# Performance work log

Hardware: AMD Instinct MI355X
Metric: run time of the kernel (lower is better)

Reference implementation:

```python
import jax, jax.numpy as jnp
import numpy as np

B, S, IN, OUT = 64, 512, 256, 256   # batch, seq_len, in/out features
R, NB, E = 40, 3, 262144            # num_rels, num_bases, num_edges
N = B * S                           # total nodes in batched graph


def setup_inputs() -> dict:
    key = jax.random.key(0)
    ks = jax.random.split(key, 6)
    text = jax.random.normal(ks[0], (B, S, IN), jnp.float32)
    src = jax.random.randint(ks[1], (E,), 0, N)
    dst = jax.random.randint(ks[2], (E,), 0, N)
    rel = jax.random.randint(ks[3], (E,), 0, R)
    bases = jax.random.normal(ks[4], (NB, IN, OUT), jnp.float32) / np.sqrt(IN).astype(np.float32)
    comp = jax.random.normal(ks[5], (R, NB), jnp.float32)
    bias = jnp.zeros((OUT,), jnp.float32)
    return dict(text=text, src=src, dst=dst, rel=rel, bases=bases, comp=comp, bias=bias)


def reference(text, src, dst, rel, bases, comp, bias):
    Bt, St, INt = text.shape
    h = text.reshape(-1, INt)                       # [N, in] flattened node feats
    n_nodes = h.shape[0]
    # project every node through every basis once: [N, num_bases, out]
    t = jnp.einsum('ni,bio->nbo', h, bases)
    # per-edge message: sum_b comp[rel_e, b] * (h_src @ basis_b)  -> [E, out]
    msg = jnp.einsum('eb,ebo->eo', comp[rel], t[src])
    # scatter-sum aggregation to destination nodes
    agg = jax.ops.segment_sum(msg, dst, num_segments=n_nodes)   # [N, out]
    out = jax.nn.relu(agg + bias)
    return out.reshape(Bt, -1, out.shape[-1])
```

## Files before the change

kernel.cpp:

```cpp
#include <hip/hip_runtime.h>
#include <cstdint>

#define N_NODES 32768
#define IN_F    256
#define OUT_F   256
#define NBASES  3
#define N_EDGES 262144
#define K_DIM   (NBASES * IN_F)

typedef __attribute__((ext_vector_type(8))) short bf16x8;
typedef __attribute__((ext_vector_type(4))) float f32x4;

__device__ __forceinline__ unsigned short f2bf(float x) {
    union { float f; unsigned int u; } c; c.f = x;
    unsigned int u = c.u;
    u = (u + 0x7FFFu + ((u >> 16) & 1u)) >> 16;
    return (unsigned short)u;
}
__device__ __forceinline__ float bf2f(unsigned short h) {
    union { unsigned int u; float f; } c; c.u = ((unsigned int)h) << 16;
    return c.f;
}

__device__ __forceinline__ void async_copy16(const void* g, void* l) {
    __builtin_amdgcn_global_load_lds(
        (const __attribute__((address_space(1))) unsigned int*)g,
        (__attribute__((address_space(3))) unsigned int*)l, 16, 0, 0);
}

__global__ __launch_bounds__(256) void prep_kernel(
    const float* __restrict__ text,
    const float* __restrict__ bases,
    unsigned short* __restrict__ hb,
    unsigned short* __restrict__ Wt)
{
    const int tid = threadIdx.x;
    if (blockIdx.x < 8192) {
        if (!hb) return;
        int i = blockIdx.x * 256 + tid;
        float4 v = reinterpret_cast<const float4*>(text)[i];
        ushort4 o;
        o.x = f2bf(v.x); o.y = f2bf(v.y); o.z = f2bf(v.z); o.w = f2bf(v.w);
        reinterpret_cast<ushort4*>(hb)[i] = o;
    } else {
        int tb = blockIdx.x - 8192;
        int kb = tb % 24, ob = tb / 24;
        __shared__ float tile[32][33];
        int c = tid & 31, r8 = tid >> 5;
        #pragma unroll
        for (int i = 0; i < 4; ++i) {
            int r = r8 + 8 * i;
            tile[r][c] = bases[(size_t)(kb * 32 + r) * OUT_F + ob * 32 + c];
        }
        __syncthreads();
        #pragma unroll
        for (int i = 0; i < 4; ++i) {
            int r = r8 + 8 * i;
            Wt[(size_t)(ob * 32 + r) * K_DIM + kb * 32 + c] = f2bf(tile[c][r]);
        }
    }
}

__global__ __launch_bounds__(256) void hist_kernel(
    const int* __restrict__ dst, int* __restrict__ counts)
{
    int e = blockIdx.x * 256 + threadIdx.x;
    atomicAdd(&counts[dst[e]], 1);
}

__global__ __launch_bounds__(1024) void scan_kernel(
    int* __restrict__ counts,
    int* __restrict__ offsets)
{
    __shared__ int wsum[16];
    const int tid = threadIdx.x;
    const int wave = tid >> 6, lane = tid & 63;
    const int base = tid * 32;
    int local[32];
    int sum = 0;
    #pragma unroll
    for (int k = 0; k < 32; ++k) { local[k] = counts[base + k]; sum += local[k]; }
    int inc = sum;
    #pragma unroll
    for (int off = 1; off < 64; off <<= 1) {
        int v = __shfl_up(inc, off);
        if (lane >= off) inc += v;
    }
    if (lane == 63) wsum[wave] = inc;
    __syncthreads();
    if (wave == 0 && lane < 16) {
        int v = wsum[lane];
        #pragma unroll
        for (int off = 1; off < 16; off <<= 1) {
            int u = __shfl_up(v, off);
            if (lane >= off) v += u;
        }
        wsum[lane] = v;
    }
    __syncthreads();
    int run = inc - sum + (wave ? wsum[wave - 1] : 0);
    #pragma unroll
    for (int k = 0; k < 32; ++k) {
        offsets[base + k] = run;
        counts[base + k] = run;
        run += local[k];
    }
    if (tid == 1023) offsets[N_NODES] = run;
}

__global__ __launch_bounds__(256) void scatter_kernel(
    const int* __restrict__ dst, const int* __restrict__ src,
    const int* __restrict__ rel, int* __restrict__ cursor,
    int* __restrict__ packed)
{
    int e = blockIdx.x * 256 + threadIdx.x;
    int pos = atomicAdd(&cursor[dst[e]], 1);
    packed[pos] = (rel[e] << 16) | src[e];
}

__global__ __launch_bounds__(256) void agg_bf16_kernel(
    const unsigned short* __restrict__ hb,
    const int* __restrict__ packed,
    const int* __restrict__ offsets,
    const float* __restrict__ comp,
    unsigned short* __restrict__ z)
{
    __shared__ float compS[128];
    if (threadIdx.x < 120) compS[threadIdx.x] = comp[threadIdx.x];
    __syncthreads();

    const int node = blockIdx.x * 4 + (threadIdx.x >> 6);
    const int lane = threadIdx.x & 63;
    const int start = offsets[node];
    const int end   = offsets[node + 1];

    float a0[4] = {}, a1[4] = {}, a2[4] = {};

    for (int cb = start; cb < end; cb += 64) {
        int idx = cb + lane;
        int pv = (idx < end) ? packed[idx] : 0;
        int cnt = min(64, end - cb);
        int j = 0;
        for (; j + 2 <= cnt; j += 2) {
            int p0 = __shfl(pv, j);
            int p1 = __shfl(pv, j + 1);
            int s0 = p0 & 0xFFFF, r0 = p0 >> 16;
            int s1 = p1 & 0xFFFF, r1 = p1 >> 16;
            ushort4 u0 = *reinterpret_cast<const ushort4*>(
                hb + (size_t)s0 * IN_F + lane * 4);
            ushort4 u1 = *reinterpret_cast<const ushort4*>(
                hb + (size_t)s1 * IN_F + lane * 4);
            float c00 = compS[r0*3], c01 = compS[r0*3+1], c02 = compS[r0*3+2];
            float c10 = compS[r1*3], c11 = compS[r1*3+1], c12 = compS[r1*3+2];
            float v0[4] = { bf2f(u0.x), bf2f(u0.y), bf2f(u0.z), bf2f(u0.w) };
            float v1[4] = { bf2f(u1.x), bf2f(u1.y), bf2f(u1.z), bf2f(u1.w) };
            #pragma unroll
            for (int k = 0; k < 4; ++k) {
                a0[k] += c00 * v0[k] + c10 * v1[k];
                a1[k] += c01 * v0[k] + c11 * v1[k];
                a2[k] += c02 * v0[k] + c12 * v1[k];
            }
        }
        if (j < cnt) {
            int p0 = __shfl(pv, j);
            int s0 = p0 & 0xFFFF, r0 = p0 >> 16;
            ushort4 u0 = *reinterpret_cast<const ushort4*>(
                hb + (size_t)s0 * IN_F + lane * 4);
            float c00 = compS[r0*3], c01 = compS[r0*3+1], c02 = compS[r0*3+2];
            float v0[4] = { bf2f(u0.x), bf2f(u0.y), bf2f(u0.z), bf2f(u0.w) };
            #pragma unroll
            for (int k = 0; k < 4; ++k) {
                a0[k] += c00 * v0[k];
                a1[k] += c01 * v0[k];
                a2[k] += c02 * v0[k];
            }
        }
    }

    unsigned short* zp = z + (size_t)node * K_DIM + lane * 4;
    ushort4 o;
    o.x = f2bf(a0[0]); o.y = f2bf(a0[1]); o.z = f2bf(a0[2]); o.w = f2bf(a0[3]);
    *reinterpret_cast<ushort4*>(zp) = o;
    o.x = f2bf(a1[0]); o.y = f2bf(a1[1]); o.z = f2bf(a1[2]); o.w = f2bf(a1[3]);
    *reinterpret_cast<ushort4*>(zp + 256) = o;
    o.x = f2bf(a2[0]); o.y = f2bf(a2[1]); o.z = f2bf(a2[2]); o.w = f2bf(a2[3]);
    *reinterpret_cast<ushort4*>(zp + 512) = o;
}

__global__ __launch_bounds__(256) void agg_f32_kernel(
    const float* __restrict__ h,
    const int* __restrict__ packed,
    const int* __restrict__ offsets,
    const float* __restrict__ comp,
    unsigned short* __restrict__ z)
{
    __shared__ float compS[128];
    if (threadIdx.x < 120) compS[threadIdx.x] = comp[threadIdx.x];
    __syncthreads();
    const int node = blockIdx.x * 4 + (threadIdx.x >> 6);
    const int lane = threadIdx.x & 63;
    const int start = offsets[node];
    const int end   = offsets[node + 1];
    float a0[4] = {}, a1[4] = {}, a2[4] = {};
    for (int cb = start; cb < end; cb += 64) {
        int idx = cb + lane;
        int pv = (idx < end) ? packed[idx] : 0;
        int cnt = min(64, end - cb);
        for (int j = 0; j < cnt; ++j) {
            int p = __shfl(pv, j);
            int s = p & 0xFFFF, r = p >> 16;
            float c0 = compS[r*3], c1 = compS[r*3+1], c2 = compS[r*3+2];
            float4 v = *reinterpret_cast<const float4*>(
                h + (size_t)s * IN_F + lane * 4);
            a0[0] += c0*v.x; a0[1] += c0*v.y; a0[2] += c0*v.z; a0[3] += c0*v.w;
            a1[0] += c1*v.x; a1[1] += c1*v.y; a1[2] += c1*v.z; a1[3] += c1*v.w;
            a2[0] += c2*v.x; a2[1] += c2*v.y; a2[2] += c2*v.z; a2[3] += c2*v.w;
        }
    }
    unsigned short* zp = z + (size_t)node * K_DIM + lane * 4;
    ushort4 o;
    o.x = f2bf(a0[0]); o.y = f2bf(a0[1]); o.z = f2bf(a0[2]); o.w = f2bf(a0[3]);
    *reinterpret_cast<ushort4*>(zp) = o;
    o.x = f2bf(a1[0]); o.y = f2bf(a1[1]); o.z = f2bf(a1[2]); o.w = f2bf(a1[3]);
    *reinterpret_cast<ushort4*>(zp + 256) = o;
    o.x = f2bf(a2[0]); o.y = f2bf(a2[1]); o.z = f2bf(a2[2]); o.w = f2bf(a2[3]);
    *reinterpret_cast<ushort4*>(zp + 512) = o;
}

__global__ __launch_bounds__(256) void gemm_kernel(
    const unsigned short* __restrict__ A,
    const unsigned short* __restrict__ Bt,
    const float* __restrict__ bias,
    float* __restrict__ out)
{
    __shared__ __align__(16) unsigned short As[128 * 32];
    __shared__ __align__(16) unsigned short Bs[128 * 32];

    const int tid  = threadIdx.x;
    const int wave = tid >> 6, lane = tid & 63;
    const int quad = lane >> 4, l16 = lane & 15;
    const int wm = (wave & 1) * 64, wn = (wave >> 1) * 64;
    const int m0 = blockIdx.x * 128, n0 = blockIdx.y * 128;

    f32x4 acc[4][4] = {};

    const unsigned short *ga[2], *gb[2];
    unsigned short *la[2], *lb[2];
    #pragma unroll
    for (int c = 0; c < 2; ++c) {
        int p = c * 256 + wave * 64 + lane;
        int row = p >> 2;
        int oct = (p & 3) ^ ((row >> 1) & 3);
        ga[c] = A  + (size_t)(m0 + row) * K_DIM + oct * 8;
        gb[c] = Bt + (size_t)(n0 + row) * K_DIM + oct * 8;
        la[c] = As + (size_t)(c * 256 + wave * 64) * 8;
        lb[c] = Bs + (size_t)(c * 256 + wave * 64) * 8;
    }

    for (int k0 = 0; k0 < K_DIM; k0 += 32) {
        async_copy16(ga[0] + k0, la[0]);
        async_copy16(ga[1] + k0, la[1]);
        async_copy16(gb[0] + k0, lb[0]);
        async_copy16(gb[1] + k0, lb[1]);
        __syncthreads();

        bf16x8 af[4], bfr[4];
        #pragma unroll
        for (int i = 0; i < 4; ++i) {
            int row = wm + i * 16 + l16;
            int oph = quad ^ ((row >> 1) & 3);
            af[i] = *reinterpret_cast<const bf16x8*>(&As[(row * 4 + oph) * 8]);
            int nn   = wn + i * 16 + l16;
            int oph2 = quad ^ ((nn >> 1) & 3);
            bfr[i] = *reinterpret_cast<const bf16x8*>(&Bs[(nn * 4 + oph2) * 8]);
        }
        #pragma unroll
        for (int i = 0; i < 4; ++i)
            #pragma unroll
            for (int j = 0; j < 4; ++j)
                acc[i][j] = __builtin_amdgcn_mfma_f32_16x16x32_bf16(
                    af[i], bfr[j], acc[i][j], 0, 0, 0);
        __syncthreads();
    }

    #pragma unroll
    for (int j = 0; j < 4; ++j) {
        int col = n0 + wn + j * 16 + l16;
        float bv = bias[col];
        #pragma unroll
        for (int i = 0; i < 4; ++i) {
            int row_base = m0 + wm + i * 16 + quad * 4;
            #pragma unroll
            for (int r = 0; r < 4; ++r)
                out[(size_t)(row_base + r) * OUT_F + col] =
                    fmaxf(acc[i][j][r] + bv, 0.f);
        }
    }
}

extern "C" void kernel_launch(void* const* d_in, const int* in_sizes, int n_in,
                              void* d_out, int out_size, void* d_ws, size_t ws_size,
                              hipStream_t stream) {
    const float* text  = (const float*)d_in[0];
    const int*   src   = (const int*)d_in[1];
    const int*   dst   = (const int*)d_in[2];
    const int*   rel   = (const int*)d_in[3];
    const float* bases = (const float*)d_in[4];
    const float* comp  = (const float*)d_in[5];
    const float* bias  = (const float*)d_in[6];
    float* out = (float*)d_out;

    char* p = (char*)d_ws;
    unsigned short* z = (unsigned short*)p;       p += (size_t)N_NODES * K_DIM * 2;
    int* packed  = (int*)p;                       p += (size_t)N_EDGES * 4;
    int* offsets = (int*)p;                       p += (size_t)(N_NODES + 4) * 4;
    int* counts  = (int*)p;                       p += (size_t)N_NODES * 4;
    unsigned short* Wt = (unsigned short*)p;      p += (size_t)OUT_F * K_DIM * 2;
    bool use_bf16_h = (ws_size >= (size_t)(p - (char*)d_ws) + (size_t)N_NODES * IN_F * 2);
    unsigned short* hb = use_bf16_h ? (unsigned short*)p : nullptr;

    hipMemsetAsync(counts, 0, (size_t)N_NODES * sizeof(int), stream);

    prep_kernel<<<8384, 256, 0, stream>>>(text, bases, hb, Wt);
    hist_kernel<<<N_EDGES / 256, 256, 0, stream>>>(dst, counts);
    scan_kernel<<<1, 1024, 0, stream>>>(counts, offsets);
    scatter_kernel<<<N_EDGES / 256, 256, 0, stream>>>(dst, src, rel, counts, packed);
    if (use_bf16_h)
        agg_bf16_kernel<<<N_NODES / 4, 256, 0, stream>>>(hb, packed, offsets, comp, z);
    else
        agg_f32_kernel<<<N_NODES / 4, 256, 0, stream>>>(text, packed, offsets, comp, z);
    gemm_kernel<<<dim3(N_NODES / 128, OUT_F / 128), 256, 0, stream>>>(
        z, Wt, bias, out);
}
```

Baseline: 187.8 us.

## Double-buffer GEMM tiles, vectorize edge kernels, fold memset into prep kernel

The GEMM now uses 64x128 tiles with double-buffered LDS, so the next K-slice's async copy is issued before computing on the current one, and there is one barrier per step instead of two. The histogram and scatter kernels each read four edges per thread with int4 loads, the scan loads counts as int4, and the counts memset moves into extra blocks of the prep kernel to save a launch. The aggregation inner loop handles four edges per iteration with masked coefficients so more gathers are in flight. Together these target latency stalls, launch overhead and the GEMM's single-buffered load/compute serialization, at the cost of more registers, more LDS and extra masked work on tail edges.

```diff
diff --git a/kernel.cpp b/kernel.cpp
--- a/kernel.cpp
+++ b/kernel.cpp
@@ -32,7 +32,8 @@
     const float* __restrict__ text,
     const float* __restrict__ bases,
     unsigned short* __restrict__ hb,
-    unsigned short* __restrict__ Wt)
+    unsigned short* __restrict__ Wt,
+    int* __restrict__ counts)
 {
     const int tid = threadIdx.x;
     if (blockIdx.x < 8192) {
@@ -42,7 +43,7 @@
         ushort4 o;
         o.x = f2bf(v.x); o.y = f2bf(v.y); o.z = f2bf(v.z); o.w = f2bf(v.w);
         reinterpret_cast<ushort4*>(hb)[i] = o;
-    } else {
+    } else if (blockIdx.x < 8384) {
         int tb = blockIdx.x - 8192;
         int kb = tb % 24, ob = tb / 24;
         __shared__ float tile[32][33];
@@ -58,14 +59,21 @@
             int r = r8 + 8 * i;
             Wt[(size_t)(ob * 32 + r) * K_DIM + kb * 32 + c] = f2bf(tile[c][r]);
         }
+    } else {
+        int i = (blockIdx.x - 8384) * 256 + tid;
+        counts[i] = 0;
     }
 }
 
 __global__ __launch_bounds__(256) void hist_kernel(
     const int* __restrict__ dst, int* __restrict__ counts)
 {
-    int e = blockIdx.x * 256 + threadIdx.x;
-    atomicAdd(&counts[dst[e]], 1);
+    int e4 = blockIdx.x * 256 + threadIdx.x;
+    int4 d = reinterpret_cast<const int4*>(dst)[e4];
+    atomicAdd(&counts[d.x], 1);
+    atomicAdd(&counts[d.y], 1);
+    atomicAdd(&counts[d.z], 1);
+    atomicAdd(&counts[d.w], 1);
 }
 
 __global__ __launch_bounds__(1024) void scan_kernel(
@@ -79,7 +87,12 @@
     int local[32];
     int sum = 0;
     #pragma unroll
-    for (int k = 0; k < 32; ++k) { local[k] = counts[base + k]; sum += local[k]; }
+    for (int k8 = 0; k8 < 8; ++k8) {
+        int4 v = reinterpret_cast<const int4*>(counts + base)[k8];
+        local[k8 * 4 + 0] = v.x; local[k8 * 4 + 1] = v.y;
+        local[k8 * 4 + 2] = v.z; local[k8 * 4 + 3] = v.w;
+        sum += v.x + v.y + v.z + v.w;
+    }
     int inc = sum;
     #pragma unroll
     for (int off = 1; off < 64; off <<= 1) {
@@ -113,9 +126,18 @@
     const int* __restrict__ rel, int* __restrict__ cursor,
     int* __restrict__ packed)
 {
-    int e = blockIdx.x * 256 + threadIdx.x;
-    int pos = atomicAdd(&cursor[dst[e]], 1);
-    packed[pos] = (rel[e] << 16) | src[e];
+    int e4 = blockIdx.x * 256 + threadIdx.x;
+    int4 d = reinterpret_cast<const int4*>(dst)[e4];
+    int4 s = reinterpret_cast<const int4*>(src)[e4];
+    int4 r = reinterpret_cast<const int4*>(rel)[e4];
+    int p0 = atomicAdd(&cursor[d.x], 1);
+    packed[p0] = (r.x << 16) | s.x;
+    int p1 = atomicAdd(&cursor[d.y], 1);
+    packed[p1] = (r.y << 16) | s.y;
+    int p2 = atomicAdd(&cursor[d.z], 1);
+    packed[p2] = (r.z << 16) | s.z;
+    int p3 = atomicAdd(&cursor[d.w], 1);
+    packed[p3] = (r.w << 16) | s.w;
 }
 
 __global__ __launch_bounds__(256) void agg_bf16_kernel(
@@ -140,39 +162,30 @@
         int idx = cb + lane;
         int pv = (idx < end) ? packed[idx] : 0;
         int cnt = min(64, end - cb);
-        int j = 0;
-        for (; j + 2 <= cnt; j += 2) {
-            int p0 = __shfl(pv, j);
-            int p1 = __shfl(pv, j + 1);
-            int s0 = p0 & 0xFFFF, r0 = p0 >> 16;
-            int s1 = p1 & 0xFFFF, r1 = p1 >> 16;
-            ushort4 u0 = *reinterpret_cast<const ushort4*>(
-                hb + (size_t)s0 * IN_F + lane * 4);
-            ushort4 u1 = *reinterpret_cast<const ushort4*>(
-                hb + (size_t)s1 * IN_F + lane * 4);
-            float c00 = compS[r0*3], c01 = compS[r0*3+1], c02 = compS[r0*3+2];
-            float c10 = compS[r1*3], c11 = compS[r1*3+1], c12 = compS[r1*3+2];
-            float v0[4] = { bf2f(u0.x), bf2f(u0.y), bf2f(u0.z), bf2f(u0.w) };
-            float v1[4] = { bf2f(u1.x), bf2f(u1.y), bf2f(u1.z), bf2f(u1.w) };
+        for (int j = 0; j < cnt; j += 4) {
+            float c0[4], c1[4], c2[4];
+            ushort4 u[4];
             #pragma unroll
-            for (int k = 0; k < 4; ++k) {
-                a0[k] += c00 * v0[k] + c10 * v1[k];
-                a1[k] += c01 * v0[k] + c11 * v1[k];
-                a2[k] += c02 * v0[k] + c12 * v1[k];
+            for (int q = 0; q < 4; ++q) {
+                int p = __shfl(pv, j + q);
+                int s = p & 0xFFFF, r = p >> 16;
+                float m = (j + q < cnt) ? 1.f : 0.f;
+                c0[q] = m * compS[r * 3 + 0];
+                c1[q] = m * compS[r * 3 + 1];
+                c2[q] = m * compS[r * 3 + 2];
+                u[q] = *reinterpret_cast<const ushort4*>(
+                    hb + (size_t)s * IN_F + lane * 4);
             }
-        }
-        if (j < cnt) {
-            int p0 = __shfl(pv, j);
-            int s0 = p0 & 0xFFFF, r0 = p0 >> 16;
-            ushort4 u0 = *reinterpret_cast<const ushort4*>(
-                hb + (size_t)s0 * IN_F + lane * 4);
-            float c00 = compS[r0*3], c01 = compS[r0*3+1], c02 = compS[r0*3+2];
-            float v0[4] = { bf2f(u0.x), bf2f(u0.y), bf2f(u0.z), bf2f(u0.w) };
             #pragma unroll
-            for (int k = 0; k < 4; ++k) {
-                a0[k] += c00 * v0[k];
-                a1[k] += c01 * v0[k];
-                a2[k] += c02 * v0[k];
+            for (int q = 0; q < 4; ++q) {
+                float v[4] = { bf2f(u[q].x), bf2f(u[q].y),
+                               bf2f(u[q].z), bf2f(u[q].w) };
+                #pragma unroll
+                for (int k = 0; k < 4; ++k) {
+                    a0[k] += c0[q] * v[k];
+                    a1[k] += c1[q] * v[k];
+                    a2[k] += c2[q] * v[k];
+                }
             }
         }
     }
@@ -233,54 +246,68 @@
     const float* __restrict__ bias,
     float* __restrict__ out)
 {
-    __shared__ __align__(16) unsigned short As[128 * 32];
-    __shared__ __align__(16) unsigned short Bs[128 * 32];
+    __shared__ __align__(16) unsigned short As[2][64 * 32];
+    __shared__ __align__(16) unsigned short Bs[2][128 * 32];
 
     const int tid  = threadIdx.x;
     const int wave = tid >> 6, lane = tid & 63;
     const int quad = lane >> 4, l16 = lane & 15;
-    const int wm = (wave & 1) * 64, wn = (wave >> 1) * 64;
-    const int m0 = blockIdx.x * 128, n0 = blockIdx.y * 128;
-
-    f32x4 acc[4][4] = {};
-
-    const unsigned short *ga[2], *gb[2];
-    unsigned short *la[2], *lb[2];
+    const int wm = (wave & 1) * 32, wn = (wave >> 1) * 64;
+    const int m0 = blockIdx.x * 64, n0 = blockIdx.y * 128;
+
+    f32x4 acc[2][4] = {};
+
+    const int pa   = wave * 64 + lane;
+    const int rowa = pa >> 2;
+    const int octa = (pa & 3) ^ ((rowa >> 1) & 3);
+    const unsigned short* ga = A + (size_t)(m0 + rowa) * K_DIM + octa * 8;
+    const int la_off = (wave * 64) * 8;
+
+    const unsigned short* gb[2];
+    int lb_off[2];
     #pragma unroll
     for (int c = 0; c < 2; ++c) {
-        int p = c * 256 + wave * 64 + lane;
+        int p   = c * 256 + wave * 64 + lane;
         int row = p >> 2;
         int oct = (p & 3) ^ ((row >> 1) & 3);
-        ga[c] = A  + (size_t)(m0 + row) * K_DIM + oct * 8;
         gb[c] = Bt + (size_t)(n0 + row) * K_DIM + oct * 8;
-        la[c] = As + (size_t)(c * 256 + wave * 64) * 8;
-        lb[c] = Bs + (size_t)(c * 256 + wave * 64) * 8;
-    }
-
-    for (int k0 = 0; k0 < K_DIM; k0 += 32) {
-        async_copy16(ga[0] + k0, la[0]);
-        async_copy16(ga[1] + k0, la[1]);
-        async_copy16(gb[0] + k0, lb[0]);
-        async_copy16(gb[1] + k0, lb[1]);
+        lb_off[c] = (c * 256 + wave * 64) * 8;
+    }
+
+    async_copy16(ga, &As[0][la_off]);
+    async_copy16(gb[0], &Bs[0][lb_off[0]]);
+    async_copy16(gb[1], &Bs[0][lb_off[1]]);
+
+    int cur = 0;
+    for (int step = 0; step < K_DIM / 32; ++step) {
         __syncthreads();
-
-        bf16x8 af[4], bfr[4];
-        #pragma unroll
-        for (int i = 0; i < 4; ++i) {
+        int k1 = (step + 1) * 32;
+        if (k1 < K_DIM) {
+            async_copy16(ga + k1, &As[cur ^ 1][la_off]);
+            async_copy16(gb[0] + k1, &Bs[cur ^ 1][lb_off[0]]);
+            async_copy16(gb[1] + k1, &Bs[cur ^ 1][lb_off[1]]);
+        }
+
+        bf16x8 af[2], bfr[4];
+        #pragma unroll
+        for (int i = 0; i < 2; ++i) {
             int row = wm + i * 16 + l16;
             int oph = quad ^ ((row >> 1) & 3);
-            af[i] = *reinterpret_cast<const bf16x8*>(&As[(row * 4 + oph) * 8]);
-            int nn   = wn + i * 16 + l16;
+            af[i] = *reinterpret_cast<const bf16x8*>(&As[cur][(row * 4 + oph) * 8]);
+        }
+        #pragma unroll
+        for (int j = 0; j < 4; ++j) {
+            int nn   = wn + j * 16 + l16;
             int oph2 = quad ^ ((nn >> 1) & 3);
-            bfr[i] = *reinterpret_cast<const bf16x8*>(&Bs[(nn * 4 + oph2) * 8]);
-        }
-        #pragma unroll
-        for (int i = 0; i < 4; ++i)
+            bfr[j] = *reinterpret_cast<const bf16x8*>(&Bs[cur][(nn * 4 + oph2) * 8]);
+        }
+        #pragma unroll
+        for (int i = 0; i < 2; ++i)
             #pragma unroll
             for (int j = 0; j < 4; ++j)
                 acc[i][j] = __builtin_amdgcn_mfma_f32_16x16x32_bf16(
                     af[i], bfr[j], acc[i][j], 0, 0, 0);
-        __syncthreads();
+        cur ^= 1;
     }
 
     #pragma unroll
@@ -288,7 +315,7 @@
         int col = n0 + wn + j * 16 + l16;
         float bv = bias[col];
         #pragma unroll
-        for (int i = 0; i < 4; ++i) {
+        for (int i = 0; i < 2; ++i) {
             int row_base = m0 + wm + i * 16 + quad * 4;
             #pragma unroll
             for (int r = 0; r < 4; ++r)
@@ -319,16 +346,14 @@
     bool use_bf16_h = (ws_size >= (size_t)(p - (char*)d_ws) + (size_t)N_NODES * IN_F * 2);
     unsigned short* hb = use_bf16_h ? (unsigned short*)p : nullptr;
 
-    hipMemsetAsync(counts, 0, (size_t)N_NODES * sizeof(int), stream);
-
-    prep_kernel<<<8384, 256, 0, stream>>>(text, bases, hb, Wt);
-    hist_kernel<<<N_EDGES / 256, 256, 0, stream>>>(dst, counts);
+    prep_kernel<<<8512, 256, 0, stream>>>(text, bases, hb, Wt, counts);
+    hist_kernel<<<N_EDGES / 1024, 256, 0, stream>>>(dst, counts);
     scan_kernel<<<1, 1024, 0, stream>>>(counts, offsets);
-    scatter_kernel<<<N_EDGES / 256, 256, 0, stream>>>(dst, src, rel, counts, packed);
+    scatter_kernel<<<N_EDGES / 1024, 256, 0, stream>>>(dst, src, rel, counts, packed);
     if (use_bf16_h)
         agg_bf16_kernel<<<N_NODES / 4, 256, 0, stream>>>(hb, packed, offsets, comp, z);
     else
         agg_f32_kernel<<<N_NODES / 4, 256, 0, stream>>>(text, packed, offsets, comp, z);
-    gemm_kernel<<<dim3(N_NODES / 128, OUT_F / 128), 256, 0, stream>>>(
+    gemm_kernel<<<dim3(N_NODES / 64, OUT_F / 128), 256, 0, stream>>>(
         z, Wt, bias, out);
 }
```

Measured after the change: 193.4 us. 3.0% more time.
